# Kernel tuning notes

Hardware: AMD Instinct MI355X
Metric: run time of the kernel (lower is better)

The kernel has to match this reference:

```python
import jax, jax.numpy as jnp
import numpy as np

B, T, H = 32, 2048, 1024


def setup_inputs() -> dict:
    key = jax.random.key(0)
    k1, k2, k3, k4, k5 = jax.random.split(key, 5)
    hidden = jax.random.normal(k1, (1, B, H), dtype=jnp.float32)
    encoder_outputs = jax.random.normal(k2, (B, T, H), dtype=jnp.float32)
    # nn.Linear(2H, H): weight [H, 2H], bias [H]
    lim = 1.0 / np.sqrt(2 * H)
    W = jax.random.uniform(k3, (H, 2 * H), minval=-lim, maxval=lim, dtype=jnp.float32)
    b = jax.random.uniform(k4, (H,), minval=-lim, maxval=lim, dtype=jnp.float32)
    stdv = 1.0 / np.sqrt(H)
    v = jax.random.uniform(k5, (H,), minval=-stdv, maxval=stdv, dtype=jnp.float32)
    return {"hidden": hidden, "encoder_outputs": encoder_outputs, "W": W, "b": b, "v": v}


def reference(hidden, encoder_outputs, W, b, v):
    # hidden: [1, B, H] -> broadcast to [B, T, H]
    h = jnp.broadcast_to(jnp.transpose(hidden, (1, 0, 2)), encoder_outputs.shape)
    x = jnp.concatenate([h, encoder_outputs], axis=2)          # [B, T, 2H]
    energy = jnp.tanh(jnp.einsum('btd,hd->bth', x, W) + b)      # [B, T, H]
    scores = jnp.einsum('h,bth->bt', v, energy)[:, None, :]     # [B, 1, T]
    return jax.nn.softmax(scores, axis=2)
```

## Files before the change

kernel.cpp:

```cpp
#include <hip/hip_runtime.h>
#include <hip/hip_bf16.h>

#define H 1024
#define T 2048
#define B 32
#define BM 128
#define BKC 64
#define NCHUNK 16
#define NCOLT 2
#define BCOLS 512

typedef __attribute__((ext_vector_type(8))) __bf16 bf16x8;
typedef __attribute__((ext_vector_type(16))) float f32x16;
typedef __attribute__((ext_vector_type(8))) unsigned short u16x8;

__device__ __forceinline__ unsigned short f2bf(float f) {
    unsigned int x = __float_as_uint(f);
    x += 0x7fffu + ((x >> 16) & 1u);
    return (unsigned short)(x >> 16);
}

__device__ __forceinline__ float fast_tanh(float x) {
    float t = __expf(2.0f * x);
    return 1.0f - 2.0f * __builtin_amdgcn_rcpf(t + 1.0f);
}

__global__ __launch_bounds__(256) void prep_w_kernel(const float* __restrict__ W,
                                                     unsigned short* __restrict__ Wp) {
    int gid = blockIdx.x * 256 + threadIdx.x;
    int n = gid & (H - 1);
    int kg = gid >> 10;
    const float* srcp = W + (size_t)n * (2 * H) + H + kg * 8;
    float4 f0 = *(const float4*)(srcp);
    float4 f1 = *(const float4*)(srcp + 4);
    u16x8 o;
    o[0] = f2bf(f0.x); o[1] = f2bf(f0.y); o[2] = f2bf(f0.z); o[3] = f2bf(f0.w);
    o[4] = f2bf(f1.x); o[5] = f2bf(f1.y); o[6] = f2bf(f1.z); o[7] = f2bf(f1.w);
    *(u16x8*)(Wp + (size_t)gid * 8) = o;
}

__global__ __launch_bounds__(128) void prep_hp_kernel(const float* __restrict__ hidden,
                                                      const float* __restrict__ W,
                                                      const float* __restrict__ bias,
                                                      float* __restrict__ hp) {
    int b = blockIdx.y;
    int h = blockIdx.x * 128 + threadIdx.x;
    const float* hid = hidden + (size_t)b * H;
    const float* wr = W + (size_t)h * (2 * H);
    float acc = 0.f;
    for (int d = 0; d < H; d += 4) {
        float4 wv = *(const float4*)(wr + d);
        float4 hv = *(const float4*)(hid + d);
        acc += wv.x * hv.x + wv.y * hv.y + wv.z * hv.z + wv.w * hv.w;
    }
    hp[(size_t)b * H + h] = acc + bias[h];
}

#define MFMA32(A, Bv, C) __builtin_amdgcn_mfma_f32_32x32x16_bf16(A, Bv, C, 0, 0, 0)

__global__ __launch_bounds__(1024, 4) void energy_kernel(const float* __restrict__ enc,
                                                         const float* __restrict__ hp,
                                                         const float* __restrict__ vvec,
                                                         const unsigned short* __restrict__ Wp,
                                                         float* __restrict__ sc_part) {
    __shared__ __align__(16) unsigned short Abuf[2][BM * BKC];
    __shared__ float scpart[16][BM];

    const int tid = threadIdx.x;
    const int b = blockIdx.z;
    const int t0 = blockIdx.x * BM;
    const int c0 = blockIdx.y * BCOLS;
    const int wave = tid >> 6;
    const int lane = tid & 63;
    const int l31 = lane & 31;
    const int hi = lane >> 5;

    const int st_ks = tid & 7;
    const int st_row = tid >> 3;
    const float* st_src = enc + ((size_t)b * T + t0 + st_row) * H + st_ks * 8;
    char* Ab0 = (char*)&Abuf[0][0];
    char* st_dst = Ab0 + st_ks * 2048 + (((st_row ^ st_ks)) << 4);

    const unsigned short* wp_base = Wp + (size_t)(c0 + wave * 32 + l31) * 8 + (size_t)hi * (H * 8);

    f32x16 acc[4];
#pragma unroll
    for (int rg = 0; rg < 4; ++rg)
#pragma unroll
        for (int i = 0; i < 16; ++i) acc[rg][i] = 0.f;

    const int rv0 = 0 * 32 + l31;
    const int rv1 = 1 * 32 + l31;
    const int rv2 = 2 * 32 + l31;
    const int rv3 = 3 * 32 + l31;

    {
        float4 f0 = *(const float4*)(st_src);
        float4 f1 = *(const float4*)(st_src + 4);
        u16x8 o;
        o[0] = f2bf(f0.x); o[1] = f2bf(f0.y); o[2] = f2bf(f0.z); o[3] = f2bf(f0.w);
        o[4] = f2bf(f1.x); o[5] = f2bf(f1.y); o[6] = f2bf(f1.z); o[7] = f2bf(f1.w);
        *(u16x8*)st_dst = o;
    }
    bf16x8 bfA = *(const bf16x8*)(wp_base);
    bf16x8 bfB = *(const bf16x8*)(wp_base + (size_t)1 * (H * 16));
    __syncthreads();

#define STEP(KI, BF)                                                          \
    {                                                                          \
        const int kslot = (KI) * 2 + hi;                                       \
        const char* ap = Ab + kslot * 2048;                                    \
        bf16x8 a0 = *(const bf16x8*)(ap + ((rv0 ^ kslot) << 4));               \
        bf16x8 a1 = *(const bf16x8*)(ap + ((rv1 ^ kslot) << 4));               \
        bf16x8 a2 = *(const bf16x8*)(ap + ((rv2 ^ kslot) << 4));               \
        bf16x8 a3 = *(const bf16x8*)(ap + ((rv3 ^ kslot) << 4));               \
        acc[0] = MFMA32(a0, BF, acc[0]);                                       \
        acc[1] = MFMA32(a1, BF, acc[1]);                                       \
        acc[2] = MFMA32(a2, BF, acc[2]);                                       \
        acc[3] = MFMA32(a3, BF, acc[3]);                                       \
        const int nit = j * 4 + (KI) + 2;                                      \
        if (nit < 64) BF = *(const bf16x8*)(wp_base + (size_t)nit * (H * 16)); \
    }

    for (int j = 0; j < NCHUNK; ++j) {
        float4 f0, f1;
        const bool pfA = (j < NCHUNK - 1);
        if (pfA) {
            const float* p = st_src + (j + 1) * BKC;
            f0 = *(const float4*)(p);
            f1 = *(const float4*)(p + 4);
        }
        const char* Ab = Ab0 + (j & 1) * 16384;
        STEP(0, bfA)
        STEP(1, bfB)
        STEP(2, bfA)
        STEP(3, bfB)
        if (pfA) {
            u16x8 o;
            o[0] = f2bf(f0.x); o[1] = f2bf(f0.y); o[2] = f2bf(f0.z); o[3] = f2bf(f0.w);
            o[4] = f2bf(f1.x); o[5] = f2bf(f1.y); o[6] = f2bf(f1.z); o[7] = f2bf(f1.w);
            *(u16x8*)(st_dst + ((j + 1) & 1) * 16384) = o;
        }
        __syncthreads();
    }
#undef STEP

    const size_t bH = (size_t)b * H;
    const int col = c0 + wave * 32 + l31;
    const float hpv = hp[bH + col];
    const float vv = vvec[col];
    float psc[4][16];
#pragma unroll
    for (int rg = 0; rg < 4; ++rg)
#pragma unroll
        for (int r = 0; r < 16; ++r)
            psc[rg][r] = vv * fast_tanh(acc[rg][r] + hpv);

#pragma unroll
    for (int rg = 0; rg < 4; ++rg)
#pragma unroll
        for (int r = 0; r < 16; ++r) {
            float s = psc[rg][r];
            s += __shfl_xor(s, 1);
            s += __shfl_xor(s, 2);
            s += __shfl_xor(s, 4);
            s += __shfl_xor(s, 8);
            s += __shfl_xor(s, 16);
            psc[rg][r] = s;
        }
    if (l31 == 0) {
#pragma unroll
        for (int rg = 0; rg < 4; ++rg)
#pragma unroll
            for (int r = 0; r < 16; ++r) {
                int m = rg * 32 + (r & 3) + 8 * (r >> 2) + 4 * hi;
                scpart[wave][m] = psc[rg][r];
            }
    }
    __syncthreads();
    if (tid < BM) {
        float s = 0.f;
#pragma unroll
        for (int w = 0; w < 16; ++w) s += scpart[w][tid];
        sc_part[((size_t)blockIdx.y * B + b) * T + t0 + tid] = s;
    }
}

__global__ __launch_bounds__(256) void softmax_kernel(const float* __restrict__ sc,
                                                      float* __restrict__ out) {
    int b = blockIdx.x;
    int tid = threadIdx.x;
    int wave = tid >> 6, lane = tid & 63;
    const float* row0 = sc + (size_t)b * T;
    const float* row1 = sc + ((size_t)B + b) * T;
    float vals[8];
    float m = -1e30f;
#pragma unroll
    for (int i = 0; i < 8; ++i) {
        int idx = tid + 256 * i;
        vals[i] = row0[idx] + row1[idx];
        m = fmaxf(m, vals[i]);
    }
#pragma unroll
    for (int s = 1; s < 64; s <<= 1) m = fmaxf(m, __shfl_xor(m, s));
    __shared__ float red[4];
    __shared__ float red2[4];
    if (lane == 0) red[wave] = m;
    __syncthreads();
    m = fmaxf(fmaxf(red[0], red[1]), fmaxf(red[2], red[3]));
    float sum = 0.f;
#pragma unroll
    for (int i = 0; i < 8; ++i) { vals[i] = expf(vals[i] - m); sum += vals[i]; }
#pragma unroll
    for (int s = 1; s < 64; s <<= 1) sum += __shfl_xor(sum, s);
    if (lane == 0) red2[wave] = sum;
    __syncthreads();
    sum = red2[0] + red2[1] + red2[2] + red2[3];
    float inv = 1.0f / sum;
#pragma unroll
    for (int i = 0; i < 8; ++i) out[(size_t)b * T + tid + 256 * i] = vals[i] * inv;
}

extern "C" void kernel_launch(void* const* d_in, const int* in_sizes, int n_in,
                              void* d_out, int out_size, void* d_ws, size_t ws_size,
                              hipStream_t stream) {
    (void)in_sizes; (void)n_in; (void)out_size; (void)ws_size;
    const float* hidden = (const float*)d_in[0];
    const float* enc    = (const float*)d_in[1];
    const float* W      = (const float*)d_in[2];
    const float* bias   = (const float*)d_in[3];
    const float* v      = (const float*)d_in[4];
    float* out = (float*)d_out;

    unsigned short* Wp = (unsigned short*)d_ws;
    float* hp = (float*)((char*)d_ws + 2 * 1024 * 1024);
    float* sc = (float*)((char*)d_ws + 2 * 1024 * 1024 + 128 * 1024);

    prep_w_kernel<<<dim3(512), dim3(256), 0, stream>>>(W, Wp);
    prep_hp_kernel<<<dim3(8, B), dim3(128), 0, stream>>>(hidden, W, bias, hp);
    energy_kernel<<<dim3(T / BM, NCOLT, B), dim3(1024), 0, stream>>>(enc, hp, v, Wp, sc);
    softmax_kernel<<<dim3(B), dim3(256), 0, stream>>>(sc, out);
}
```

Before: 275.0 us.

## Retile energy GEMM to 2x2 wave tiles with 256-column blocks

Each energy block now covers 256 output columns with 512 threads, arranged as a 2x4 grid of waves that each compute a 64x64 tile (2x2 MFMA accumulators) instead of a 128x32 strip. The goal is better register reuse of A and B fragments per MFMA, with fewer LDS reads per MFMA. It also adds s_setprio around the MFMA group and makes the softmax sum four column-block partials. The cost is that the encoder tile is loaded and converted twice as many times overall, since there are now four column blocks per row tile.

Result: faster. 258.6 us (-6.0%).

```diff
diff --git a/kernel.cpp b/kernel.cpp
--- a/kernel.cpp
+++ b/kernel.cpp
@@ -7,8 +7,8 @@
 #define BM 128
 #define BKC 64
 #define NCHUNK 16
-#define NCOLT 2
-#define BCOLS 512
+#define NCOLT 4
+#define BCOLS 256
 
 typedef __attribute__((ext_vector_type(8))) __bf16 bf16x8;
 typedef __attribute__((ext_vector_type(16))) float f32x16;
@@ -58,13 +58,13 @@
 
 #define MFMA32(A, Bv, C) __builtin_amdgcn_mfma_f32_32x32x16_bf16(A, Bv, C, 0, 0, 0)
 
-__global__ __launch_bounds__(1024, 4) void energy_kernel(const float* __restrict__ enc,
-                                                         const float* __restrict__ hp,
-                                                         const float* __restrict__ vvec,
-                                                         const unsigned short* __restrict__ Wp,
-                                                         float* __restrict__ sc_part) {
+__global__ __launch_bounds__(512, 4) void energy_kernel(const float* __restrict__ enc,
+                                                        const float* __restrict__ hp,
+                                                        const float* __restrict__ vvec,
+                                                        const unsigned short* __restrict__ Wp,
+                                                        float* __restrict__ sc_part) {
     __shared__ __align__(16) unsigned short Abuf[2][BM * BKC];
-    __shared__ float scpart[16][BM];
+    __shared__ float scpart[8][BM];
 
     const int tid = threadIdx.x;
     const int b = blockIdx.z;
@@ -74,90 +74,109 @@
     const int lane = tid & 63;
     const int l31 = lane & 31;
     const int hi = lane >> 5;
-
-    const int st_ks = tid & 7;
-    const int st_row = tid >> 3;
-    const float* st_src = enc + ((size_t)b * T + t0 + st_row) * H + st_ks * 8;
+    const int wr = wave >> 2;
+    const int wc = wave & 3;
+
+    const int st_row = tid >> 2;
+    const int st_kq = tid & 3;
+    const int ks0 = st_kq * 2, ks1 = ks0 + 1;
+    const float* st_src = enc + ((size_t)b * T + t0 + st_row) * H + st_kq * 16;
     char* Ab0 = (char*)&Abuf[0][0];
-    char* st_dst = Ab0 + st_ks * 2048 + (((st_row ^ st_ks)) << 4);
-
-    const unsigned short* wp_base = Wp + (size_t)(c0 + wave * 32 + l31) * 8 + (size_t)hi * (H * 8);
-
-    f32x16 acc[4];
-#pragma unroll
-    for (int rg = 0; rg < 4; ++rg)
-#pragma unroll
-        for (int i = 0; i < 16; ++i) acc[rg][i] = 0.f;
-
-    const int rv0 = 0 * 32 + l31;
-    const int rv1 = 1 * 32 + l31;
-    const int rv2 = 2 * 32 + l31;
-    const int rv3 = 3 * 32 + l31;
+    char* st_d0 = Ab0 + ks0 * 2048 + (((st_row ^ ks0)) << 4);
+    char* st_d1 = Ab0 + ks1 * 2048 + (((st_row ^ ks1)) << 4);
+
+    const unsigned short* wp_base = Wp + (size_t)(c0 + wc * 64 + l31) * 8 + (size_t)hi * (H * 8);
+
+    f32x16 acc00, acc01, acc10, acc11;
+#pragma unroll
+    for (int i = 0; i < 16; ++i) { acc00[i] = 0.f; acc01[i] = 0.f; acc10[i] = 0.f; acc11[i] = 0.f; }
+
+    const int rv0 = wr * 64 + l31;
+    const int rv1 = wr * 64 + 32 + l31;
 
     {
         float4 f0 = *(const float4*)(st_src);
         float4 f1 = *(const float4*)(st_src + 4);
-        u16x8 o;
-        o[0] = f2bf(f0.x); o[1] = f2bf(f0.y); o[2] = f2bf(f0.z); o[3] = f2bf(f0.w);
-        o[4] = f2bf(f1.x); o[5] = f2bf(f1.y); o[6] = f2bf(f1.z); o[7] = f2bf(f1.w);
-        *(u16x8*)st_dst = o;
-    }
-    bf16x8 bfA = *(const bf16x8*)(wp_base);
-    bf16x8 bfB = *(const bf16x8*)(wp_base + (size_t)1 * (H * 16));
-    __syncthreads();
-
-#define STEP(KI, BF)                                                          \
+        float4 f2 = *(const float4*)(st_src + 8);
+        float4 f3 = *(const float4*)(st_src + 12);
+        u16x8 o0, o1;
+        o0[0] = f2bf(f0.x); o0[1] = f2bf(f0.y); o0[2] = f2bf(f0.z); o0[3] = f2bf(f0.w);
+        o0[4] = f2bf(f1.x); o0[5] = f2bf(f1.y); o0[6] = f2bf(f1.z); o0[7] = f2bf(f1.w);
+        o1[0] = f2bf(f2.x); o1[1] = f2bf(f2.y); o1[2] = f2bf(f2.z); o1[3] = f2bf(f2.w);
+        o1[4] = f2bf(f3.x); o1[5] = f2bf(f3.y); o1[6] = f2bf(f3.z); o1[7] = f2bf(f3.w);
+        *(u16x8*)st_d0 = o0;
+        *(u16x8*)st_d1 = o1;
+    }
+    bf16x8 bA0 = *(const bf16x8*)(wp_base);
+    bf16x8 bA1 = *(const bf16x8*)(wp_base + 256);
+    bf16x8 bB0 = *(const bf16x8*)(wp_base + (size_t)1 * (H * 16));
+    bf16x8 bB1 = *(const bf16x8*)(wp_base + (size_t)1 * (H * 16) + 256);
+    __syncthreads();
+
+#define STEP(KI, C0, C1)                                                       \
     {                                                                          \
         const int kslot = (KI) * 2 + hi;                                       \
         const char* ap = Ab + kslot * 2048;                                    \
         bf16x8 a0 = *(const bf16x8*)(ap + ((rv0 ^ kslot) << 4));               \
         bf16x8 a1 = *(const bf16x8*)(ap + ((rv1 ^ kslot) << 4));               \
-        bf16x8 a2 = *(const bf16x8*)(ap + ((rv2 ^ kslot) << 4));               \
-        bf16x8 a3 = *(const bf16x8*)(ap + ((rv3 ^ kslot) << 4));               \
-        acc[0] = MFMA32(a0, BF, acc[0]);                                       \
-        acc[1] = MFMA32(a1, BF, acc[1]);                                       \
-        acc[2] = MFMA32(a2, BF, acc[2]);                                       \
-        acc[3] = MFMA32(a3, BF, acc[3]);                                       \
+        __builtin_amdgcn_s_setprio(1);                                         \
+        acc00 = MFMA32(a0, C0, acc00);                                         \
+        acc01 = MFMA32(a0, C1, acc01);                                         \
+        acc10 = MFMA32(a1, C0, acc10);                                         \
+        acc11 = MFMA32(a1, C1, acc11);                                         \
+        __builtin_amdgcn_s_setprio(0);                                         \
         const int nit = j * 4 + (KI) + 2;                                      \
-        if (nit < 64) BF = *(const bf16x8*)(wp_base + (size_t)nit * (H * 16)); \
+        if (nit < 64) {                                                        \
+            const unsigned short* bp = wp_base + (size_t)nit * (H * 16);       \
+            C0 = *(const bf16x8*)(bp);                                         \
+            C1 = *(const bf16x8*)(bp + 256);                                   \
+        }                                                                      \
     }
 
     for (int j = 0; j < NCHUNK; ++j) {
-        float4 f0, f1;
+        float4 f0, f1, f2, f3;
         const bool pfA = (j < NCHUNK - 1);
         if (pfA) {
             const float* p = st_src + (j + 1) * BKC;
             f0 = *(const float4*)(p);
             f1 = *(const float4*)(p + 4);
+            f2 = *(const float4*)(p + 8);
+            f3 = *(const float4*)(p + 12);
         }
         const char* Ab = Ab0 + (j & 1) * 16384;
-        STEP(0, bfA)
-        STEP(1, bfB)
-        STEP(2, bfA)
-        STEP(3, bfB)
+        STEP(0, bA0, bA1)
+        STEP(1, bB0, bB1)
+        STEP(2, bA0, bA1)
+        STEP(3, bB0, bB1)
         if (pfA) {
-            u16x8 o;
-            o[0] = f2bf(f0.x); o[1] = f2bf(f0.y); o[2] = f2bf(f0.z); o[3] = f2bf(f0.w);
-            o[4] = f2bf(f1.x); o[5] = f2bf(f1.y); o[6] = f2bf(f1.z); o[7] = f2bf(f1.w);
-            *(u16x8*)(st_dst + ((j + 1) & 1) * 16384) = o;
+            u16x8 o0, o1;
+            o0[0] = f2bf(f0.x); o0[1] = f2bf(f0.y); o0[2] = f2bf(f0.z); o0[3] = f2bf(f0.w);
+            o0[4] = f2bf(f1.x); o0[5] = f2bf(f1.y); o0[6] = f2bf(f1.z); o0[7] = f2bf(f1.w);
+            o1[0] = f2bf(f2.x); o1[1] = f2bf(f2.y); o1[2] = f2bf(f2.z); o1[3] = f2bf(f2.w);
+            o1[4] = f2bf(f3.x); o1[5] = f2bf(f3.y); o1[6] = f2bf(f3.z); o1[7] = f2bf(f3.w);
+            char* d0 = st_d0 + ((j + 1) & 1) * 16384;
+            char* d1 = st_d1 + ((j + 1) & 1) * 16384;
+            *(u16x8*)d0 = o0;
+            *(u16x8*)d1 = o1;
         }
         __syncthreads();
     }
 #undef STEP
 
     const size_t bH = (size_t)b * H;
-    const int col = c0 + wave * 32 + l31;
-    const float hpv = hp[bH + col];
-    const float vv = vvec[col];
-    float psc[4][16];
-#pragma unroll
-    for (int rg = 0; rg < 4; ++rg)
-#pragma unroll
-        for (int r = 0; r < 16; ++r)
-            psc[rg][r] = vv * fast_tanh(acc[rg][r] + hpv);
-
-#pragma unroll
-    for (int rg = 0; rg < 4; ++rg)
+    const int col0 = c0 + wc * 64 + l31;
+    const int col1 = col0 + 32;
+    const float hp0 = hp[bH + col0], hp1 = hp[bH + col1];
+    const float v0 = vvec[col0], v1 = vvec[col1];
+    float psc[2][16];
+#pragma unroll
+    for (int r = 0; r < 16; ++r) {
+        psc[0][r] = v0 * fast_tanh(acc00[r] + hp0) + v1 * fast_tanh(acc01[r] + hp1);
+        psc[1][r] = v0 * fast_tanh(acc10[r] + hp0) + v1 * fast_tanh(acc11[r] + hp1);
+    }
+
+#pragma unroll
+    for (int rg = 0; rg < 2; ++rg)
 #pragma unroll
         for (int r = 0; r < 16; ++r) {
             float s = psc[rg][r];
@@ -170,18 +189,18 @@
         }
     if (l31 == 0) {
 #pragma unroll
-        for (int rg = 0; rg < 4; ++rg)
+        for (int rg = 0; rg < 2; ++rg)
 #pragma unroll
             for (int r = 0; r < 16; ++r) {
-                int m = rg * 32 + (r & 3) + 8 * (r >> 2) + 4 * hi;
+                int m = wr * 64 + rg * 32 + (r & 3) + 8 * (r >> 2) + 4 * hi;
                 scpart[wave][m] = psc[rg][r];
             }
     }
     __syncthreads();
     if (tid < BM) {
-        float s = 0.f;
-#pragma unroll
-        for (int w = 0; w < 16; ++w) s += scpart[w][tid];
+        const int wbase = (tid >> 6) * 4;
+        float s = scpart[wbase][tid] + scpart[wbase + 1][tid] +
+                  scpart[wbase + 2][tid] + scpart[wbase + 3][tid];
         sc_part[((size_t)blockIdx.y * B + b) * T + t0 + tid] = s;
     }
 }
@@ -191,14 +210,16 @@
     int b = blockIdx.x;
     int tid = threadIdx.x;
     int wave = tid >> 6, lane = tid & 63;
-    const float* row0 = sc + (size_t)b * T;
-    const float* row1 = sc + ((size_t)B + b) * T;
+    const float* r0 = sc + (size_t)b * T;
+    const float* r1 = sc + ((size_t)B + b) * T;
+    const float* r2 = sc + ((size_t)2 * B + b) * T;
+    const float* r3 = sc + ((size_t)3 * B + b) * T;
     float vals[8];
     float m = -1e30f;
 #pragma unroll
     for (int i = 0; i < 8; ++i) {
         int idx = tid + 256 * i;
-        vals[i] = row0[idx] + row1[idx];
+        vals[i] = (r0[idx] + r1[idx]) + (r2[idx] + r3[idx]);
         m = fmaxf(m, vals[i]);
     }
 #pragma unroll
@@ -238,6 +259,6 @@
 
     prep_w_kernel<<<dim3(512), dim3(256), 0, stream>>>(W, Wp);
     prep_hp_kernel<<<dim3(8, B), dim3(128), 0, stream>>>(hidden, W, bias, hp);
-    energy_kernel<<<dim3(T / BM, NCOLT, B), dim3(1024), 0, stream>>>(enc, hp, v, Wp, sc);
+    energy_kernel<<<dim3(T / BM, NCOLT, B), dim3(512), 0, stream>>>(enc, hp, v, Wp, sc);
     softmax_kernel<<<dim3(B), dim3(256), 0, stream>>>(sc, out);
 }
```
